# Optimization experiments

Measured on AMD Instinct MI355X. Metric: run time of the kernel, lower is better.

The kernel has to match this reference:

```python
import jax, jax.numpy as jnp
import numpy as np

N = 10000
E = 320000
IN_DIM = 256
HID = 128
HEADS = 3
NEG_SLOPE = 0.2
EPS = 1e-8


def setup_inputs() -> dict:
    key = jax.random.key(0)
    ks = jax.random.split(key, 12)
    rn = lambda k, s, sc=0.1: jax.random.normal(k, s, dtype=jnp.float32) * sc
    return {
        'x1': jax.random.normal(ks[0], (N, IN_DIM), dtype=jnp.float32),
        'edge_index1': jax.random.randint(ks[1], (2, E), 0, N, dtype=jnp.int64),
        'x2': jax.random.normal(ks[2], (N, IN_DIM), dtype=jnp.float32),
        'edge_index2': jax.random.randint(ks[3], (2, E), 0, N, dtype=jnp.int64),
        'W1': rn(ks[4], (IN_DIM, HEADS * HID)),
        'att_src1': rn(ks[5], (HEADS, HID)),
        'att_dst1': rn(ks[6], (HEADS, HID)),
        'b1': rn(ks[7], (HEADS * HID,)),
        'W2': rn(ks[8], (HEADS * HID, HID)),
        'att_src2': rn(ks[9], (1, HID)),
        'att_dst2': rn(ks[10], (1, HID)),
        'b2': rn(ks[11], (HID,)),
    }


def gat_conv(x, edge_index, W, a_src, a_dst, bias, heads, out_ch, concat):
    """PyG-style GATConv with add_self_loops=True."""
    n = x.shape[0]
    loops = jnp.arange(n, dtype=edge_index.dtype)
    ei = jnp.concatenate([edge_index, jnp.stack([loops, loops])], axis=1)
    src, dst = ei[0], ei[1]
    h = (x @ W).reshape(n, heads, out_ch)                    # [N,H,C]
    s = jnp.einsum('nhc,hc->nh', h, a_src)                    # alpha_src per node
    d = jnp.einsum('nhc,hc->nh', h, a_dst)                    # alpha_dst per node
    e = jax.nn.leaky_relu(s[src] + d[dst], NEG_SLOPE)         # [Etot,H]
    m = jax.ops.segment_max(e, dst, num_segments=n)           # segment softmax (stable)
    ex = jnp.exp(e - m[dst])
    denom = jax.ops.segment_sum(ex, dst, num_segments=n)
    alpha = ex / denom[dst]                                   # [Etot,H]
    out = jax.ops.segment_sum(h[src] * alpha[:, :, None], dst, num_segments=n)
    out = out.reshape(n, heads * out_ch) if concat else out.mean(axis=1)
    return out + bias, (ei, alpha)


def _branch(x, ei, W1, as1, ad1, b1, W2, as2, ad2, b2):
    e1, (ei_sl, alpha1) = gat_conv(x, ei, W1, as1, ad1, b1, HEADS, HID, True)
    e1 = jax.nn.relu(e1)
    e2, _ = gat_conv(e1, ei, W2, as2, ad2, b2, 1, HID, False)
    # _graph_pooling
    attn_val = alpha1.mean(axis=1)                            # [Etot]
    node_attn = jax.ops.segment_sum(attn_val, ei_sl[1], num_segments=x.shape[0])
    weighted = e2 * node_attn[:, None]
    pooled = jnp.concatenate([weighted.mean(axis=0), e2.mean(axis=0)])  # [2*HID]
    return pooled, alpha1


def reference(x1, edge_index1, x2, edge_index2, W1, att_src1, att_dst1, b1,
              W2, att_src2, att_dst2, b2):
    g1, alpha1 = _branch(x1, edge_index1, W1, att_src1, att_dst1, b1,
                         W2, att_src2, att_dst2, b2)
    g2, alpha2 = _branch(x2, edge_index2, W1, att_src1, att_dst1, b1,
                         W2, att_src2, att_dst2, b2)
    n1 = jnp.maximum(jnp.linalg.norm(g1), EPS)
    n2 = jnp.maximum(jnp.linalg.norm(g2), EPS)
    sim = jnp.dot(g1, g2) / (n1 * n2)
    return sim, alpha1, alpha2
```

## Files before the change

kernel.cpp:

```cpp
#include <hip/hip_runtime.h>
#include <hip/hip_bf16.h>
#include <cstdint>
#include <cstddef>

#define INDIM 256
#define NEG 0.2f

typedef __attribute__((ext_vector_type(8))) short short8v;
typedef __attribute__((ext_vector_type(4))) float f32x4;
typedef __attribute__((ext_vector_type(2))) float f32x2;

__device__ __forceinline__ unsigned short f2bf(float x) {
  __hip_bfloat16 b = __float2bfloat16(x);
  return __builtin_bit_cast(unsigned short, b);
}

__device__ __forceinline__ unsigned char f2fp8(float v) {
  int packed = __builtin_amdgcn_cvt_pk_fp8_f32(v, v, 0, false);
  return (unsigned char)(packed & 0xff);
}

__device__ __forceinline__ float lrelu(float v) { return v > 0.f ? v : NEG * v; }

__global__ void wprep_kernel(const float* __restrict__ W, __hip_bfloat16* __restrict__ Wt,
                             int K, int NC, int total) {
  int idx = blockIdx.x * blockDim.x + threadIdx.x;
  if (idx >= total) return;
  int k = idx / NC, c = idx - k * NC;
  Wt[(size_t)c * K + k] = __float2bfloat16(W[idx]);
}

template<int K, bool ABF16>
__global__ __launch_bounds__(256) void mfma_gemm(const void* __restrict__ A0,
                                                 const void* __restrict__ A1, int Nsplit,
                                                 const __hip_bfloat16* __restrict__ Wt,
                                                 float* __restrict__ Y,
                                                 unsigned char* __restrict__ Yc,
                                                 int M, int NC) {
  __shared__ short As[64][40];
  __shared__ short Bs[128][40];
  const int tid = threadIdx.x;
  const int row0 = blockIdx.x * 64;
  const int col0 = blockIdx.y * 128;
  const int l = tid & 63, w = tid >> 6;
  const int wr = w >> 1, wc = w & 1;
  const int lr = l & 15, lk = (l >> 4) * 8;

  f32x4 acc[2][4];
#pragma unroll
  for (int m = 0; m < 2; ++m)
#pragma unroll
    for (int n = 0; n < 4; ++n) acc[m][n] = {0.f, 0.f, 0.f, 0.f};

  for (int k0 = 0; k0 < K; k0 += 32) {
    __syncthreads();
    {
      int r = tid >> 2, kq = (tid & 3) * 8;
      int gr = row0 + r;
      short8v av = {0, 0, 0, 0, 0, 0, 0, 0};
      if (gr < M) {
        const void* Ab = (gr < Nsplit) ? A0 : A1;
        int lrow = (gr < Nsplit) ? gr : gr - Nsplit;
        if (ABF16) {
          av = *(const short8v*)((const short*)Ab + (size_t)lrow * K + k0 + kq);
        } else {
          const float* ap = (const float*)Ab + (size_t)lrow * K + k0 + kq;
          float4 u = *(const float4*)ap;
          float4 v = *(const float4*)(ap + 4);
          av = short8v{(short)f2bf(u.x), (short)f2bf(u.y), (short)f2bf(u.z), (short)f2bf(u.w),
                       (short)f2bf(v.x), (short)f2bf(v.y), (short)f2bf(v.z), (short)f2bf(v.w)};
        }
      }
      *(short8v*)&As[r][kq] = av;
    }
    {
      int c = tid >> 1, kq = (tid & 1) * 8;
      const short* wp = (const short*)Wt + (size_t)(col0 + c) * K + k0 + kq;
      *(short8v*)&Bs[c][kq]      = *(const short8v*)wp;
      *(short8v*)&Bs[c][kq + 16] = *(const short8v*)(wp + 16);
    }
    __syncthreads();
    short8v a[2], b[4];
#pragma unroll
    for (int m = 0; m < 2; ++m) a[m] = *(short8v*)&As[wr * 32 + m * 16 + lr][lk];
#pragma unroll
    for (int n = 0; n < 4; ++n) b[n] = *(short8v*)&Bs[wc * 64 + n * 16 + lr][lk];
#pragma unroll
    for (int m = 0; m < 2; ++m)
#pragma unroll
      for (int n = 0; n < 4; ++n)
        acc[m][n] = __builtin_amdgcn_mfma_f32_16x16x32_bf16(a[m], b[n], acc[m][n], 0, 0, 0);
  }
#pragma unroll
  for (int m = 0; m < 2; ++m) {
    int rbase = row0 + wr * 32 + m * 16 + (l >> 4) * 4;
#pragma unroll
    for (int n = 0; n < 4; ++n) {
      int col = col0 + wc * 64 + n * 16 + lr;
#pragma unroll
      for (int q = 0; q < 4; ++q) {
        int row = rbase + q;
        if (row < M) {
          float v = acc[m][n][q];
          Y[(size_t)row * NC + col] = v;
          Yc[(size_t)row * NC + col] = f2fp8(v);
        }
      }
    }
  }
}

__global__ __launch_bounds__(256) void sd_kernel(const float* __restrict__ H,
                                                 const float* __restrict__ As,
                                                 const float* __restrict__ Ad,
                                                 float* __restrict__ S, float* __restrict__ D,
                                                 int NB, int NH) {
  int w = blockIdx.x * 4 + (threadIdx.x >> 6);
  if (w >= NB) return;
  int lane = threadIdx.x & 63;
  int h = w % NH;
  float2 hv = reinterpret_cast<const float2*>(H + (size_t)w * 128)[lane];
  float2 as = reinterpret_cast<const float2*>(As + h * 128)[lane];
  float2 ad = reinterpret_cast<const float2*>(Ad + h * 128)[lane];
  float vs = hv.x * as.x + hv.y * as.y;
  float vd = hv.x * ad.x + hv.y * ad.y;
#pragma unroll
  for (int o = 32; o; o >>= 1) { vs += __shfl_down(vs, o); vd += __shfl_down(vd, o); }
  if (lane == 0) { S[w] = vs; D[w] = vd; }
}

__global__ void deg_kernel(const int* __restrict__ ed1, const int* __restrict__ ed2,
                           int E, int Etot, int N, int* __restrict__ deg) {
  int idx = blockIdx.x * blockDim.x + threadIdx.x;
  if (idx >= 2 * Etot) return;
  int br = idx >= Etot;
  int el = idx - br * Etot;
  const int* ed = br ? ed2 : ed1;
  int dn = ((el < E) ? ed[el] : (el - E)) + br * N;
  atomicAdd(&deg[dn], 1);
}

__global__ __launch_bounds__(1024) void scan_kernel(const int* __restrict__ deg,
                                                    int* __restrict__ rowptr,
                                                    int* __restrict__ cursor, int n) {
  __shared__ int wsum[16];
  __shared__ int carry_s;
  int tid = threadIdx.x;
  int lane = tid & 63, wid = tid >> 6;
  if (tid == 0) { carry_s = 0; rowptr[0] = 0; }
  __syncthreads();
  for (int base = 0; base < n; base += 1024) {
    int i = base + tid;
    int v = (i < n) ? deg[i] : 0;
    int x = v;
#pragma unroll
    for (int o = 1; o < 64; o <<= 1) {
      int t = __shfl_up(x, o);
      if (lane >= o) x += t;
    }
    if (lane == 63) wsum[wid] = x;
    __syncthreads();
    if (wid == 0) {
      int wv = (lane < 16) ? wsum[lane] : 0;
#pragma unroll
      for (int o = 1; o < 16; o <<= 1) {
        int t = __shfl_up(wv, o);
        if (lane >= o) wv += t;
      }
      if (lane < 16) wsum[lane] = wv;
    }
    __syncthreads();
    int incl = carry_s + (wid ? wsum[wid - 1] : 0) + x;
    if (i < n) { rowptr[i + 1] = incl; cursor[i] = incl - v; }
    __syncthreads();
    if (tid == 1023) carry_s = incl;
    __syncthreads();
  }
}

__global__ void fill_kernel(const int* __restrict__ es1, const int* __restrict__ ed1,
                            const int* __restrict__ es2, const int* __restrict__ ed2,
                            int E, int Etot, int N, int* __restrict__ cursor,
                            int* __restrict__ csr_src) {
  int idx = blockIdx.x * blockDim.x + threadIdx.x;
  if (idx >= 2 * Etot) return;
  int br = idx >= Etot;
  int el = idx - br * Etot;
  const int* es = br ? es2 : es1;
  const int* ed = br ? ed2 : ed1;
  int sn, dn;
  if (el < E) { sn = es[el]; dn = ed[el]; } else { sn = dn = el - E; }
  sn += br * N; dn += br * N;
  int pos = atomicAdd(&cursor[dn], 1);
  csr_src[pos] = sn;
}

__global__ __launch_bounds__(192) void agg1_kernel(const unsigned char* __restrict__ h1c,
                                                   const float* __restrict__ S,
                                                   const float* __restrict__ D,
                                                   const int* __restrict__ rowptr,
                                                   const int* __restrict__ csr_src,
                                                   const float* __restrict__ b1,
                                                   __hip_bfloat16* __restrict__ e1b,
                                                   float* __restrict__ invden) {
  __shared__ int lsrc[192];
  __shared__ float la[3][192];
  __shared__ float red[3][3];
  __shared__ float inv_s[3];
  const unsigned int* H4 = reinterpret_cast<const unsigned int*>(h1c);
  int n = blockIdx.x;
  int j = threadIdx.x;
  int wid = j >> 6, lane = j & 63;
  int half = (j >= 96) ? 1 : 0;
  int t = j - half * 96;
  int head = t >> 5;
  int p0 = rowptr[n], p1 = rowptr[n + 1];
  float d0 = D[n * 3], d1 = D[n * 3 + 1], d2 = D[n * 3 + 2];

  float dp0 = 0.f, dp1 = 0.f, dp2 = 0.f;
  float acc[4] = {0.f, 0.f, 0.f, 0.f};
  for (int base = p0; base < p1; base += 192) {
    int cnt = min(192, p1 - base);
    __syncthreads();
    if (j < cnt) {
      int sn = csr_src[base + j];
      lsrc[j] = sn;
      float e0 = __expf(lrelu(S[sn * 3] + d0));
      float e1 = __expf(lrelu(S[sn * 3 + 1] + d1));
      float e2 = __expf(lrelu(S[sn * 3 + 2] + d2));
      la[0][j] = e0; la[1][j] = e1; la[2][j] = e2;
      dp0 += e0; dp1 += e1; dp2 += e2;
    }
    __syncthreads();
    int i = half;
    for (; i + 14 < cnt; i += 16) {
      unsigned int hv[8];
      float av[8];
#pragma unroll
      for (int u = 0; u < 8; ++u) {
        int e = i + 2 * u;
        int sn = lsrc[e];
        av[u] = la[head][e];
        hv[u] = H4[(size_t)sn * 96 + t];
      }
#pragma unroll
      for (int u = 0; u < 8; ++u) {
        f32x2 f0 = __builtin_amdgcn_cvt_pk_f32_fp8((int)hv[u], false);
        f32x2 f1 = __builtin_amdgcn_cvt_pk_f32_fp8((int)hv[u], true);
        acc[0] = fmaf(av[u], f0.x, acc[0]);
        acc[1] = fmaf(av[u], f0.y, acc[1]);
        acc[2] = fmaf(av[u], f1.x, acc[2]);
        acc[3] = fmaf(av[u], f1.y, acc[3]);
      }
    }
    for (; i < cnt; i += 2) {
      int sn = lsrc[i];
      float a = la[head][i];
      unsigned int hv = H4[(size_t)sn * 96 + t];
      f32x2 f0 = __builtin_amdgcn_cvt_pk_f32_fp8((int)hv, false);
      f32x2 f1 = __builtin_amdgcn_cvt_pk_f32_fp8((int)hv, true);
      acc[0] = fmaf(a, f0.x, acc[0]);
      acc[1] = fmaf(a, f0.y, acc[1]);
      acc[2] = fmaf(a, f1.x, acc[2]);
      acc[3] = fmaf(a, f1.y, acc[3]);
    }
  }
  __syncthreads();
  float* racc = &la[0][0];
  if (half == 1) {
    racc[t * 4 + 0] = acc[0]; racc[t * 4 + 1] = acc[1];
    racc[t * 4 + 2] = acc[2]; racc[t * 4 + 3] = acc[3];
  }
  __syncthreads();
  if (half == 0) {
    acc[0] += racc[t * 4 + 0]; acc[1] += racc[t * 4 + 1];
    acc[2] += racc[t * 4 + 2]; acc[3] += racc[t * 4 + 3];
  }
#pragma unroll
  for (int o = 32; o; o >>= 1) {
    dp0 += __shfl_down(dp0, o); dp1 += __shfl_down(dp1, o); dp2 += __shfl_down(dp2, o);
  }
  if (lane == 0) { red[wid][0] = dp0; red[wid][1] = dp1; red[wid][2] = dp2; }
  __syncthreads();
  if (j == 0) {
    inv_s[0] = 1.f / (red[0][0] + red[1][0] + red[2][0]);
    inv_s[1] = 1.f / (red[0][1] + red[1][1] + red[2][1]);
    inv_s[2] = 1.f / (red[0][2] + red[1][2] + red[2][2]);
  }
  __syncthreads();
  if (half == 0) {
    float inv = inv_s[head];
    float4 bb = *reinterpret_cast<const float4*>(b1 + 4 * t);
    float v0 = acc[0] * inv + bb.x;
    float v1 = acc[1] * inv + bb.y;
    float v2 = acc[2] * inv + bb.z;
    float v3 = acc[3] * inv + bb.w;
    v0 = v0 > 0.f ? v0 : 0.f; v1 = v1 > 0.f ? v1 : 0.f;
    v2 = v2 > 0.f ? v2 : 0.f; v3 = v3 > 0.f ? v3 : 0.f;
    uint2 st;
    st.x = (unsigned int)f2bf(v0) | ((unsigned int)f2bf(v1) << 16);
    st.y = (unsigned int)f2bf(v2) | ((unsigned int)f2bf(v3) << 16);
    *reinterpret_cast<uint2*>(reinterpret_cast<unsigned short*>(e1b) + (size_t)n * 384 + 4 * t) = st;
  }
  if (j < 3) invden[n * 3 + j] = inv_s[j];
}

__global__ void alpha_kernel(const float* __restrict__ S, const float* __restrict__ D,
                             const float* __restrict__ invden,
                             const int* __restrict__ es1, const int* __restrict__ ed1,
                             const int* __restrict__ es2, const int* __restrict__ ed2,
                             int E, int Etot, int N, float* __restrict__ out) {
  int idx = blockIdx.x * blockDim.x + threadIdx.x;
  if (idx >= 2 * Etot) return;
  int br = idx >= Etot;
  int el = idx - br * Etot;
  const int* es = br ? es2 : es1;
  const int* ed = br ? ed2 : ed1;
  int sn, dn;
  if (el < E) { sn = es[el]; dn = ed[el]; } else { sn = dn = el - E; }
  sn += br * N; dn += br * N;
  float* ao = out + 1 + (size_t)br * Etot * 3 + (size_t)el * 3;
#pragma unroll
  for (int h = 0; h < 3; ++h) {
    float v = lrelu(S[sn * 3 + h] + D[dn * 3 + h]);
    ao[h] = __expf(v) * invden[dn * 3 + h];
  }
}

__global__ __launch_bounds__(64) void agg2_kernel(const unsigned char* __restrict__ h2c,
                                                  const float* __restrict__ S,
                                                  const float* __restrict__ D,
                                                  const int* __restrict__ rowptr,
                                                  const int* __restrict__ csr_src,
                                                  const float* __restrict__ b2,
                                                  float* __restrict__ e2out) {
  __shared__ int lsrc[256];
  __shared__ float la[256];
  const unsigned int* H4 = reinterpret_cast<const unsigned int*>(h2c);
  int n = blockIdx.x;
  int lane = threadIdx.x;
  int half = lane >> 5, t = lane & 31;
  int p0 = rowptr[n], p1 = rowptr[n + 1];
  float dn_v = D[n];

  float dpart = 0.f;
  float acc[4] = {0.f, 0.f, 0.f, 0.f};
  for (int base = p0; base < p1; base += 256) {
    int cnt = min(256, p1 - base);
    __syncthreads();
    for (int i = lane; i < cnt; i += 64) {
      int sn = csr_src[base + i];
      lsrc[i] = sn;
      float ex = __expf(lrelu(S[sn] + dn_v));
      la[i] = ex;
      dpart += ex;
    }
    __syncthreads();
    int i = half;
    for (; i + 14 < cnt; i += 16) {
      unsigned int hv[8];
      float av[8];
#pragma unroll
      for (int u = 0; u < 8; ++u) {
        int e = i + 2 * u;
        int sn = lsrc[e];
        av[u] = la[e];
        hv[u] = H4[(size_t)sn * 32 + t];
      }
#pragma unroll
      for (int u = 0; u < 8; ++u) {
        f32x2 f0 = __builtin_amdgcn_cvt_pk_f32_fp8((int)hv[u], false);
        f32x2 f1 = __builtin_amdgcn_cvt_pk_f32_fp8((int)hv[u], true);
        acc[0] = fmaf(av[u], f0.x, acc[0]);
        acc[1] = fmaf(av[u], f0.y, acc[1]);
        acc[2] = fmaf(av[u], f1.x, acc[2]);
        acc[3] = fmaf(av[u], f1.y, acc[3]);
      }
    }
    for (; i < cnt; i += 2) {
      int sn = lsrc[i];
      float a = la[i];
      unsigned int hv = H4[(size_t)sn * 32 + t];
      f32x2 f0 = __builtin_amdgcn_cvt_pk_f32_fp8((int)hv, false);
      f32x2 f1 = __builtin_amdgcn_cvt_pk_f32_fp8((int)hv, true);
      acc[0] = fmaf(a, f0.x, acc[0]);
      acc[1] = fmaf(a, f0.y, acc[1]);
      acc[2] = fmaf(a, f1.x, acc[2]);
      acc[3] = fmaf(a, f1.y, acc[3]);
    }
  }
#pragma unroll
  for (int k = 0; k < 4; ++k) acc[k] += __shfl_xor(acc[k], 32);
#pragma unroll
  for (int o = 32; o; o >>= 1) dpart += __shfl_down(dpart, o);
  float invden = 1.f / __shfl(dpart, 0);
  if (half == 0) {
    float4 bb = *reinterpret_cast<const float4*>(b2 + 4 * t);
    float4 ov;
    ov.x = acc[0] * invden + bb.x;
    ov.y = acc[1] * invden + bb.y;
    ov.z = acc[2] * invden + bb.z;
    ov.w = acc[3] * invden + bb.w;
    *reinterpret_cast<float4*>(e2out + (size_t)n * 128 + 4 * t) = ov;
  }
}

__global__ __launch_bounds__(128) void pool_kernel(const float* __restrict__ e2,
                                                   float* __restrict__ g, int N, float invN) {
  int c = threadIdx.x;
  int br = blockIdx.y;
  int r0 = br * N + blockIdx.x * 128;
  int r1 = min(r0 + 128, br * N + N);
  float acc = 0.f;
  for (int n = r0; n < r1; ++n) acc += e2[(size_t)n * 128 + c];
  acc *= invN;
  float* gb = g + (size_t)br * 256;
  atomicAdd(&gb[c], acc);
  atomicAdd(&gb[128 + c], acc);
}

__global__ __launch_bounds__(256) void sim_kernel(const float* __restrict__ g1,
                                                  const float* __restrict__ g2,
                                                  float* __restrict__ out) {
  int t = threadIdx.x;
  float a = g1[t], b = g2[t];
  __shared__ float sd[256], s1[256], s2[256];
  sd[t] = a * b; s1[t] = a * a; s2[t] = b * b;
  __syncthreads();
  for (int ofs = 128; ofs; ofs >>= 1) {
    if (t < ofs) { sd[t] += sd[t + ofs]; s1[t] += s1[t + ofs]; s2[t] += s2[t + ofs]; }
    __syncthreads();
  }
  if (t == 0) {
    float n1 = fmaxf(sqrtf(s1[0]), 1e-8f);
    float n2 = fmaxf(sqrtf(s2[0]), 1e-8f);
    out[0] = sd[0] / (n1 * n2);
  }
}

extern "C" void kernel_launch(void* const* d_in, const int* in_sizes, int n_in,
                              void* d_out, int out_size, void* d_ws, size_t ws_size,
                              hipStream_t stream) {
  const int N = in_sizes[0] / INDIM;
  const int E = in_sizes[1] / 2;
  const int Etot = E + N;
  const int N2 = 2 * N;

  const float* x1  = (const float*)d_in[0];
  const int*   ei1 = (const int*)d_in[1];
  const float* x2  = (const float*)d_in[2];
  const int*   ei2 = (const int*)d_in[3];
  const float* W1  = (const float*)d_in[4];
  const float* as1 = (const float*)d_in[5];
  const float* ad1 = (const float*)d_in[6];
  const float* b1  = (const float*)d_in[7];
  const float* W2  = (const float*)d_in[8];
  const float* as2 = (const float*)d_in[9];
  const float* ad2 = (const float*)d_in[10];
  const float* b2  = (const float*)d_in[11];
  float* out = (float*)d_out;
  const int* es1 = ei1, *ed1 = ei1 + E;
  const int* es2 = ei2, *ed2 = ei2 + E;

  char* p = (char*)d_ws;
  auto alloc = [&](size_t bytes) -> char* {
    char* q = p;
    p += (bytes + 255) & ~(size_t)255;
    return q;
  };
  float* h1          = (float*)alloc((size_t)N2 * 384 * 4);
  unsigned char* h1c = (unsigned char*)alloc((size_t)N2 * 384);
  __hip_bfloat16* e1b = (__hip_bfloat16*)alloc((size_t)N2 * 384 * 2);
  float* h2          = (float*)alloc((size_t)N2 * 128 * 4);
  unsigned char* h2c = (unsigned char*)alloc((size_t)N2 * 128);
  float* e2          = (float*)alloc((size_t)N2 * 128 * 4);
  __hip_bfloat16* W1t = (__hip_bfloat16*)alloc((size_t)256 * 384 * 2);
  __hip_bfloat16* W2t = (__hip_bfloat16*)alloc((size_t)384 * 128 * 2);
  float* s1v  = (float*)alloc((size_t)N2 * 3 * 4);
  float* d1v  = (float*)alloc((size_t)N2 * 3 * 4);
  float* s2v  = (float*)alloc((size_t)N2 * 4);
  float* d2v  = (float*)alloc((size_t)N2 * 4);
  float* idn  = (float*)alloc((size_t)N2 * 3 * 4);
  float* g    = (float*)alloc(512 * 4);
  int* deg     = (int*)alloc((size_t)N2 * 4);
  int* rowptr  = (int*)alloc((size_t)(N2 + 1) * 4);
  int* cursor  = (int*)alloc((size_t)N2 * 4);
  int* csr_src = (int*)alloc((size_t)2 * Etot * 4);

  const int EB = 256;
  const int egrid2 = (2 * Etot + EB - 1) / EB;
  const int gmx = (N2 + 63) / 64;

  hipMemsetAsync(g, 0, 512 * 4, stream);
  hipMemsetAsync(deg, 0, (size_t)N2 * 4, stream);
  wprep_kernel<<<(256 * 384 + 255) / 256, 256, 0, stream>>>(W1, W1t, 256, 384, 256 * 384);
  wprep_kernel<<<(384 * 128 + 255) / 256, 256, 0, stream>>>(W2, W2t, 384, 128, 384 * 128);

  deg_kernel<<<egrid2, EB, 0, stream>>>(ed1, ed2, E, Etot, N, deg);
  mfma_gemm<256, false><<<dim3(gmx, 3), 256, 0, stream>>>(x1, x2, N, W1t, h1, h1c, N2, 384);
  sd_kernel<<<(N2 * 3 + 3) / 4, 256, 0, stream>>>(h1, as1, ad1, s1v, d1v, N2 * 3, 3);
  scan_kernel<<<1, 1024, 0, stream>>>(deg, rowptr, cursor, N2);
  fill_kernel<<<egrid2, EB, 0, stream>>>(es1, ed1, es2, ed2, E, Etot, N, cursor, csr_src);

  agg1_kernel<<<N2, 192, 0, stream>>>(h1c, s1v, d1v, rowptr, csr_src, b1, e1b, idn);
  alpha_kernel<<<egrid2, EB, 0, stream>>>(s1v, d1v, idn, es1, ed1, es2, ed2, E, Etot, N, out);

  mfma_gemm<384, true><<<dim3(gmx, 1), 256, 0, stream>>>(e1b, e1b, N2, W2t, h2, h2c, N2, 128);
  sd_kernel<<<(N2 + 3) / 4, 256, 0, stream>>>(h2, as2, ad2, s2v, d2v, N2, 1);
  agg2_kernel<<<N2, 64, 0, stream>>>(h2c, s2v, d2v, rowptr, csr_src, b2, e2);

  pool_kernel<<<dim3((N + 127) / 128, 2), 128, 0, stream>>>(e2, g, N, 1.f / (float)N);
  sim_kernel<<<1, 256, 0, stream>>>(g, g + 256, out);
}
```

Before: 262.1 us.

## Precompute edge attention weights in CSR fill and fuse alpha output into aggregation

The CSR fill kernel now computes the three layer-1 exp attention logits per edge and stores them with the original edge id as a float4 in CSR order. The aggregation kernel reads these instead of gathering S per edge, and it writes the normalized alpha output itself, so the separate alpha kernel and the inverse-denominator buffer go away. A new pass precomputes the layer-2 edge weights in CSR order. The scan becomes a single pass with 20 elements per thread, and the two weight-prep launches are merged into one. In exchange, the edge data written and read grows (float4 per edge, a csr_dst array, a w2 array), and the alpha writes are now scattered.

```diff
diff --git a/kernel.cpp b/kernel.cpp
--- a/kernel.cpp
+++ b/kernel.cpp
@@ -22,12 +22,20 @@
 
 __device__ __forceinline__ float lrelu(float v) { return v > 0.f ? v : NEG * v; }
 
-__global__ void wprep_kernel(const float* __restrict__ W, __hip_bfloat16* __restrict__ Wt,
-                             int K, int NC, int total) {
+__global__ void wprep_kernel(const float* __restrict__ W1, __hip_bfloat16* __restrict__ W1t,
+                             const float* __restrict__ W2, __hip_bfloat16* __restrict__ W2t) {
   int idx = blockIdx.x * blockDim.x + threadIdx.x;
-  if (idx >= total) return;
-  int k = idx / NC, c = idx - k * NC;
-  Wt[(size_t)c * K + k] = __float2bfloat16(W[idx]);
+  const int T1 = 256 * 384;
+  if (idx < T1) {
+    int k = idx / 384, c = idx - k * 384;
+    W1t[(size_t)c * 256 + k] = __float2bfloat16(W1[idx]);
+  } else {
+    int i = idx - T1;
+    if (i < 384 * 128) {
+      int k = i / 128, c = i - k * 128;
+      W2t[(size_t)c * 384 + k] = __float2bfloat16(W2[i]);
+    }
+  }
 }
 
 template<int K, bool ABF16>
@@ -144,44 +152,53 @@
                                                     int* __restrict__ rowptr,
                                                     int* __restrict__ cursor, int n) {
   __shared__ int wsum[16];
-  __shared__ int carry_s;
-  int tid = threadIdx.x;
-  int lane = tid & 63, wid = tid >> 6;
-  if (tid == 0) { carry_s = 0; rowptr[0] = 0; }
-  __syncthreads();
-  for (int base = 0; base < n; base += 1024) {
-    int i = base + tid;
-    int v = (i < n) ? deg[i] : 0;
-    int x = v;
-#pragma unroll
-    for (int o = 1; o < 64; o <<= 1) {
-      int t = __shfl_up(x, o);
-      if (lane >= o) x += t;
-    }
-    if (lane == 63) wsum[wid] = x;
-    __syncthreads();
-    if (wid == 0) {
-      int wv = (lane < 16) ? wsum[lane] : 0;
-#pragma unroll
-      for (int o = 1; o < 16; o <<= 1) {
-        int t = __shfl_up(wv, o);
-        if (lane >= o) wv += t;
-      }
-      if (lane < 16) wsum[lane] = wv;
-    }
-    __syncthreads();
-    int incl = carry_s + (wid ? wsum[wid - 1] : 0) + x;
-    if (i < n) { rowptr[i + 1] = incl; cursor[i] = incl - v; }
-    __syncthreads();
-    if (tid == 1023) carry_s = incl;
-    __syncthreads();
+  int t = threadIdx.x, lane = t & 63, wid = t >> 6;
+  int start = t * 20;
+  int v[20];
+  int s = 0;
+#pragma unroll
+  for (int k = 0; k < 20; ++k) {
+    int i = start + k;
+    int d = (i < n) ? deg[i] : 0;
+    s += d;
+    v[k] = s;
+  }
+  int x = s;
+#pragma unroll
+  for (int o = 1; o < 64; o <<= 1) {
+    int tm = __shfl_up(x, o);
+    if (lane >= o) x += tm;
+  }
+  if (lane == 63) wsum[wid] = x;
+  __syncthreads();
+  if (wid == 0) {
+    int wv = (lane < 16) ? wsum[lane] : 0;
+#pragma unroll
+    for (int o = 1; o < 16; o <<= 1) {
+      int tm = __shfl_up(wv, o);
+      if (lane >= o) wv += tm;
+    }
+    if (lane < 16) wsum[lane] = wv;
+  }
+  __syncthreads();
+  int excl = (x - s) + (wid ? wsum[wid - 1] : 0);
+  if (t == 0) rowptr[0] = 0;
+#pragma unroll
+  for (int k = 0; k < 20; ++k) {
+    int i = start + k;
+    if (i < n) {
+      rowptr[i + 1] = excl + v[k];
+      cursor[i] = excl + (k ? v[k - 1] : 0);
+    }
   }
 }
 
 __global__ void fill_kernel(const int* __restrict__ es1, const int* __restrict__ ed1,
                             const int* __restrict__ es2, const int* __restrict__ ed2,
+                            const float* __restrict__ S1, const float* __restrict__ D1,
                             int E, int Etot, int N, int* __restrict__ cursor,
-                            int* __restrict__ csr_src) {
+                            int* __restrict__ csr_src, int* __restrict__ csr_dst,
+                            float4* __restrict__ w4) {
   int idx = blockIdx.x * blockDim.x + threadIdx.x;
   if (idx >= 2 * Etot) return;
   int br = idx >= Etot;
@@ -193,16 +210,30 @@
   sn += br * N; dn += br * N;
   int pos = atomicAdd(&cursor[dn], 1);
   csr_src[pos] = sn;
+  csr_dst[pos] = dn;
+  float4 w;
+  w.x = __expf(lrelu(S1[sn * 3]     + D1[dn * 3]));
+  w.y = __expf(lrelu(S1[sn * 3 + 1] + D1[dn * 3 + 1]));
+  w.z = __expf(lrelu(S1[sn * 3 + 2] + D1[dn * 3 + 2]));
+  w.w = __int_as_float(br * Etot + el);
+  w4[pos] = w;
+}
+
+__global__ void w2prep_kernel(const int* __restrict__ csr_src, const int* __restrict__ csr_dst,
+                              const float* __restrict__ S2, const float* __restrict__ D2,
+                              int total, float* __restrict__ w2) {
+  int pos = blockIdx.x * blockDim.x + threadIdx.x;
+  if (pos >= total) return;
+  w2[pos] = __expf(lrelu(S2[csr_src[pos]] + D2[csr_dst[pos]]));
 }
 
 __global__ __launch_bounds__(192) void agg1_kernel(const unsigned char* __restrict__ h1c,
-                                                   const float* __restrict__ S,
-                                                   const float* __restrict__ D,
                                                    const int* __restrict__ rowptr,
                                                    const int* __restrict__ csr_src,
+                                                   const float4* __restrict__ w4,
                                                    const float* __restrict__ b1,
                                                    __hip_bfloat16* __restrict__ e1b,
-                                                   float* __restrict__ invden) {
+                                                   float* __restrict__ out) {
   __shared__ int lsrc[192];
   __shared__ float la[3][192];
   __shared__ float red[3][3];
@@ -215,7 +246,6 @@
   int t = j - half * 96;
   int head = t >> 5;
   int p0 = rowptr[n], p1 = rowptr[n + 1];
-  float d0 = D[n * 3], d1 = D[n * 3 + 1], d2 = D[n * 3 + 2];
 
   float dp0 = 0.f, dp1 = 0.f, dp2 = 0.f;
   float acc[4] = {0.f, 0.f, 0.f, 0.f};
@@ -223,13 +253,10 @@
     int cnt = min(192, p1 - base);
     __syncthreads();
     if (j < cnt) {
-      int sn = csr_src[base + j];
-      lsrc[j] = sn;
-      float e0 = __expf(lrelu(S[sn * 3] + d0));
-      float e1 = __expf(lrelu(S[sn * 3 + 1] + d1));
-      float e2 = __expf(lrelu(S[sn * 3 + 2] + d2));
-      la[0][j] = e0; la[1][j] = e1; la[2][j] = e2;
-      dp0 += e0; dp1 += e1; dp2 += e2;
+      lsrc[j] = csr_src[base + j];
+      float4 w = w4[base + j];
+      la[0][j] = w.x; la[1][j] = w.y; la[2][j] = w.z;
+      dp0 += w.x; dp1 += w.y; dp2 += w.z;
     }
     __syncthreads();
     int i = half;
@@ -288,6 +315,7 @@
     inv_s[2] = 1.f / (red[0][2] + red[1][2] + red[2][2]);
   }
   __syncthreads();
+  float i0 = inv_s[0], i1 = inv_s[1], i2 = inv_s[2];
   if (half == 0) {
     float inv = inv_s[head];
     float4 bb = *reinterpret_cast<const float4*>(b1 + 4 * t);
@@ -302,34 +330,18 @@
     st.y = (unsigned int)f2bf(v2) | ((unsigned int)f2bf(v3) << 16);
     *reinterpret_cast<uint2*>(reinterpret_cast<unsigned short*>(e1b) + (size_t)n * 384 + 4 * t) = st;
   }
-  if (j < 3) invden[n * 3 + j] = inv_s[j];
-}
-
-__global__ void alpha_kernel(const float* __restrict__ S, const float* __restrict__ D,
-                             const float* __restrict__ invden,
-                             const int* __restrict__ es1, const int* __restrict__ ed1,
-                             const int* __restrict__ es2, const int* __restrict__ ed2,
-                             int E, int Etot, int N, float* __restrict__ out) {
-  int idx = blockIdx.x * blockDim.x + threadIdx.x;
-  if (idx >= 2 * Etot) return;
-  int br = idx >= Etot;
-  int el = idx - br * Etot;
-  const int* es = br ? es2 : es1;
-  const int* ed = br ? ed2 : ed1;
-  int sn, dn;
-  if (el < E) { sn = es[el]; dn = ed[el]; } else { sn = dn = el - E; }
-  sn += br * N; dn += br * N;
-  float* ao = out + 1 + (size_t)br * Etot * 3 + (size_t)el * 3;
-#pragma unroll
-  for (int h = 0; h < 3; ++h) {
-    float v = lrelu(S[sn * 3 + h] + D[dn * 3 + h]);
-    ao[h] = __expf(v) * invden[dn * 3 + h];
+  for (int p = p0 + j; p < p1; p += 192) {
+    float4 w = w4[p];
+    int eid = __float_as_int(w.w);
+    float* ao = out + 1 + (size_t)eid * 3;
+    ao[0] = w.x * i0;
+    ao[1] = w.y * i1;
+    ao[2] = w.z * i2;
   }
 }
 
 __global__ __launch_bounds__(64) void agg2_kernel(const unsigned char* __restrict__ h2c,
-                                                  const float* __restrict__ S,
-                                                  const float* __restrict__ D,
+                                                  const float* __restrict__ w2,
                                                   const int* __restrict__ rowptr,
                                                   const int* __restrict__ csr_src,
                                                   const float* __restrict__ b2,
@@ -341,7 +353,6 @@
   int lane = threadIdx.x;
   int half = lane >> 5, t = lane & 31;
   int p0 = rowptr[n], p1 = rowptr[n + 1];
-  float dn_v = D[n];
 
   float dpart = 0.f;
   float acc[4] = {0.f, 0.f, 0.f, 0.f};
@@ -349,9 +360,8 @@
     int cnt = min(256, p1 - base);
     __syncthreads();
     for (int i = lane; i < cnt; i += 64) {
-      int sn = csr_src[base + i];
-      lsrc[i] = sn;
-      float ex = __expf(lrelu(S[sn] + dn_v));
+      lsrc[i] = csr_src[base + i];
+      float ex = w2[base + i];
       la[i] = ex;
       dpart += ex;
     }
@@ -480,12 +490,14 @@
   float* d1v  = (float*)alloc((size_t)N2 * 3 * 4);
   float* s2v  = (float*)alloc((size_t)N2 * 4);
   float* d2v  = (float*)alloc((size_t)N2 * 4);
-  float* idn  = (float*)alloc((size_t)N2 * 3 * 4);
   float* g    = (float*)alloc(512 * 4);
   int* deg     = (int*)alloc((size_t)N2 * 4);
   int* rowptr  = (int*)alloc((size_t)(N2 + 1) * 4);
   int* cursor  = (int*)alloc((size_t)N2 * 4);
   int* csr_src = (int*)alloc((size_t)2 * Etot * 4);
+  int* csr_dst = (int*)alloc((size_t)2 * Etot * 4);
+  float4* w4   = (float4*)alloc((size_t)2 * Etot * 16);
+  float* w2    = (float*)alloc((size_t)2 * Etot * 4);
 
   const int EB = 256;
   const int egrid2 = (2 * Etot + EB - 1) / EB;
@@ -493,21 +505,21 @@
 
   hipMemsetAsync(g, 0, 512 * 4, stream);
   hipMemsetAsync(deg, 0, (size_t)N2 * 4, stream);
-  wprep_kernel<<<(256 * 384 + 255) / 256, 256, 0, stream>>>(W1, W1t, 256, 384, 256 * 384);
-  wprep_kernel<<<(384 * 128 + 255) / 256, 256, 0, stream>>>(W2, W2t, 384, 128, 384 * 128);
+  wprep_kernel<<<(256 * 384 + 384 * 128 + 255) / 256, 256, 0, stream>>>(W1, W1t, W2, W2t);
 
   deg_kernel<<<egrid2, EB, 0, stream>>>(ed1, ed2, E, Etot, N, deg);
   mfma_gemm<256, false><<<dim3(gmx, 3), 256, 0, stream>>>(x1, x2, N, W1t, h1, h1c, N2, 384);
   sd_kernel<<<(N2 * 3 + 3) / 4, 256, 0, stream>>>(h1, as1, ad1, s1v, d1v, N2 * 3, 3);
   scan_kernel<<<1, 1024, 0, stream>>>(deg, rowptr, cursor, N2);
-  fill_kernel<<<egrid2, EB, 0, stream>>>(es1, ed1, es2, ed2, E, Etot, N, cursor, csr_src);
-
-  agg1_kernel<<<N2, 192, 0, stream>>>(h1c, s1v, d1v, rowptr, csr_src, b1, e1b, idn);
-  alpha_kernel<<<egrid2, EB, 0, stream>>>(s1v, d1v, idn, es1, ed1, es2, ed2, E, Etot, N, out);
+  fill_kernel<<<egrid2, EB, 0, stream>>>(es1, ed1, es2, ed2, s1v, d1v, E, Etot, N,
+                                         cursor, csr_src, csr_dst, w4);
+
+  agg1_kernel<<<N2, 192, 0, stream>>>(h1c, rowptr, csr_src, w4, b1, e1b, out);
 
   mfma_gemm<384, true><<<dim3(gmx, 1), 256, 0, stream>>>(e1b, e1b, N2, W2t, h2, h2c, N2, 128);
   sd_kernel<<<(N2 + 3) / 4, 256, 0, stream>>>(h2, as2, ad2, s2v, d2v, N2, 1);
-  agg2_kernel<<<N2, 64, 0, stream>>>(h2c, s2v, d2v, rowptr, csr_src, b2, e2);
+  w2prep_kernel<<<egrid2, EB, 0, stream>>>(csr_src, csr_dst, s2v, d2v, 2 * Etot, w2);
+  agg2_kernel<<<N2, 64, 0, stream>>>(h2c, w2, rowptr, csr_src, b2, e2);
 
   pool_kernel<<<dim3((N + 127) / 128, 2), 128, 0, stream>>>(e2, g, N, 1.f / (float)N);
   sim_kernel<<<1, 256, 0, stream>>>(g, g + 256, out);
```

After: 261.9 us. Within noise of the previous version (-0.1%).
